# Kernel tuning notes

Hardware: AMD Instinct MI355X
Metric: run time of the kernel (lower is better)

## Reference

```python
import jax, jax.numpy as jnp
import numpy as np

N, E, F, H, O = 50000, 800000, 64, 128, 64
GRID_SIZE, SPLINE_ORDER = 3, 2


def make_grid(in_features, grid_size=GRID_SIZE, spline_order=SPLINE_ORDER, grid_range=(-1.0, 1.0)):
    h = (grid_range[1] - grid_range[0]) / grid_size
    pts = jnp.arange(-spline_order, grid_size + spline_order + 1, dtype=jnp.float32) * h + grid_range[0]
    return jnp.tile(pts[None, :], (in_features, 1))  # [in, grid_size + 2*order + 1]


def b_splines(x, grid, spline_order=SPLINE_ORDER):
    # x: [B, in], grid: [in, G+2k+1] -> bases [B, in, G+k]
    xe = x[..., None]
    bases = ((xe >= grid[:, :-1]) & (xe < grid[:, 1:])).astype(x.dtype)
    for k in range(1, spline_order + 1):
        bases = ((xe - grid[:, : -(k + 1)]) / (grid[:, k:-1] - grid[:, : -(k + 1)]) * bases[..., :-1]
                 + (grid[:, k + 1:] - xe) / (grid[:, k + 1:] - grid[:, 1:-k]) * bases[..., 1:])
    return bases


def setup_inputs() -> dict:
    key = jax.random.key(0)
    ks = jax.random.split(key, 12)
    x = jax.random.normal(ks[0], (N, F), dtype=jnp.float32)
    contexts = jax.random.normal(ks[1], (E, F), dtype=jnp.float32)
    attn = jax.random.uniform(ks[2], (E,), dtype=jnp.float32)
    seg_ids = jnp.sort(jax.random.randint(ks[3], (E,), 0, N, dtype=jnp.int32))
    s = 0.05
    Wn = jax.random.normal(ks[4], (H, F), dtype=jnp.float32) * s
    bn = jnp.zeros((H,), dtype=jnp.float32)
    Wc = jax.random.normal(ks[5], (H, F), dtype=jnp.float32) * s
    bc = jnp.zeros((H,), dtype=jnp.float32)
    Wu = jax.random.normal(ks[6], (O, H), dtype=jnp.float32) * s
    bu = jnp.zeros((O,), dtype=jnp.float32)
    n_coef = GRID_SIZE + SPLINE_ORDER
    base_w = jax.random.normal(ks[7], (O, O), dtype=jnp.float32) * s
    spline_w = jax.random.normal(ks[8], (O, O, n_coef), dtype=jnp.float32) * s
    spline_scaler = jnp.ones((O, O), dtype=jnp.float32)
    grid = make_grid(O)
    return dict(x=x, contexts=contexts, attn=attn, seg_ids=seg_ids, Wn=Wn, bn=bn,
                Wc=Wc, bc=bc, Wu=Wu, bu=bu, base_w=base_w, spline_w=spline_w,
                spline_scaler=spline_scaler, grid=grid)


def reference(x, contexts, attn, seg_ids, Wn, bn, Wc, bc, Wu, bu, base_w, spline_w, spline_scaler, grid):
    n = x.shape[0]
    # per-edge context transform, attention weighting
    ctx_t = contexts @ Wc.T + bc                      # [E, H]
    weighted = ctx_t * attn[:, None]                  # [E, H]
    seg_sum = jax.ops.segment_sum(weighted, seg_ids, num_segments=n)        # [N, H]
    deg = jax.ops.segment_sum(jnp.ones_like(attn), seg_ids, num_segments=n)  # [N]
    ctx_agg = seg_sum / jnp.maximum(deg, 1.0)[:, None]  # mean over edges per node
    x_t = x @ Wn.T + bn                               # [N, H]
    upd = (x_t + ctx_agg) @ Wu.T + bu                 # [N, O]
    # KANLinear (efficient-kan): silu base path + b-spline path
    base_out = jax.nn.silu(upd) @ base_w.T            # [N, O]
    bases = b_splines(upd, grid)                      # [N, O, G+k]
    scaled_sw = spline_w * spline_scaler[..., None]   # [O, O, G+k]
    spline_out = jnp.einsum('bik,oik->bo', bases, scaled_sw)
    kan_out = base_out + spline_out
    # nodes with no contexts keep their raw features (num_features == output_dim)
    return jnp.where(deg[:, None] > 0, kan_out, x)
```

## Files before the change

kernel.cpp:

```cpp
#include <hip/hip_runtime.h>
#include <hip/hip_bf16.h>

#define NN 50000
#define NE 800000

typedef short short8 __attribute__((ext_vector_type(8)));
typedef float f32x4 __attribute__((ext_vector_type(4)));
typedef unsigned short ushort_t;

static __device__ __forceinline__ unsigned bits(float f) { return __float_as_uint(f); }
static __device__ __forceinline__ float hi_f(float v) {
  return __uint_as_float(bits(v) & 0xFFFF0000u);
}
static __device__ __forceinline__ ushort_t hi_u(float v) { return (ushort_t)(bits(v) >> 16); }
static __device__ __forceinline__ unsigned pack_hi(float v0, float v1) {
  return (bits(v0) >> 16) | (bits(v1) & 0xFFFF0000u);
}
static __device__ __forceinline__ unsigned pack_lo(float v0, float v1) {
  float l0 = v0 - hi_f(v0), l1 = v1 - hi_f(v1);
  return (bits(l0) >> 16) | (bits(l1) & 0xFFFF0000u);
}

#define MFMA(a, b, c) __builtin_amdgcn_mfma_f32_16x16x32_bf16(a, b, c, 0, 0, 0)

__global__ __launch_bounds__(256) void kA_pack_off(
    const float* __restrict__ Wn, const float* __restrict__ Wc,
    const float* __restrict__ Wu, const float* __restrict__ base_w,
    const float* __restrict__ spline_w, const float* __restrict__ scaler,
    const int* __restrict__ seg,
    ushort_t* __restrict__ p1h, ushort_t* __restrict__ p2h,
    ushort_t* __restrict__ p3h, int* __restrict__ off) {
  int t = blockIdx.x * 256 + threadIdx.x;
  if (t < 4096) {
    int l = t & 63, lm = l & 15, lk = l >> 4;
    if (t < 2048) {
      int nt = t >> 8, ks = (t >> 6) & 3;
      int h = nt * 16 + lm;
#pragma unroll
      for (int j = 0; j < 8; ++j) {
        int f = ks * 32 + lk * 8 + j;
        float v = (f < 64) ? Wn[h * 64 + f] : Wc[h * 64 + (f - 64)];
        p1h[t * 8 + j] = hi_u(v);
      }
    }
    if (t < 1024) {
      int nt = t >> 8, ks = (t >> 6) & 3;
      int o = nt * 16 + lm;
#pragma unroll
      for (int j = 0; j < 8; ++j) {
        int hh = ks * 32 + lk * 8 + j;
        p2h[t * 8 + j] = hi_u(Wu[o * 128 + hh]);
      }
    }
    if (t < 3072) {
      int nt = t / 768, ks = (t >> 6) % 12;
      int o = nt * 16 + lm;
#pragma unroll
      for (int j = 0; j < 8; ++j) {
        int k = ks * 32 + lk * 8 + j;
        int i = k / 6, c = k % 6;
        float v = (c == 0) ? base_w[o * 64 + i]
                           : spline_w[(o * 64 + i) * 5 + (c - 1)] * scaler[o * 64 + i];
        p3h[t * 8 + j] = hi_u(v);
      }
    }
  }
  int e = t;
  if (e < NE) {
    int s1 = seg[e];
    if (e == 0) {
      for (int n = 0; n <= s1; ++n) off[n] = 0;
    } else {
      int s0 = seg[e - 1];
      for (int n = s0 + 1; n <= s1; ++n) off[n] = e;
    }
    if (e == NE - 1) {
      for (int n = s1 + 1; n <= NN; ++n) off[n] = NE;
    }
  }
}

__global__ __launch_bounds__(256) void k1_edge_agg(
    const float* __restrict__ contexts, const float* __restrict__ attn,
    const int* __restrict__ off, ushort_t* __restrict__ Sph,
    ushort_t* __restrict__ Spl, float* __restrict__ aprime,
    float* __restrict__ degw) {
  int n = blockIdx.x * 4 + (threadIdx.x >> 6);
  int lane = threadIdx.x & 63;
  if (n >= NN) return;
  int s = off[n];
  int e_end = off[n + 1];
  int deg_i = e_end - s;

  int sub = lane >> 4;
  int fq = lane & 15;
  const float4* ctx4 = (const float4*)contexts;

  float4 S = make_float4(0.f, 0.f, 0.f, 0.f);
  float A = 0.f;
  if (deg_i > 0) {
    int last = e_end - 1;
    for (int e0 = s; e0 < e_end; e0 += 16) {
      float a[4];
      float4 c[4];
#pragma unroll
      for (int u = 0; u < 4; ++u) {
        int eu = e0 + 4 * u + sub;
        a[u] = (eu < e_end) ? attn[eu] : 0.f;
        c[u] = ctx4[(size_t)min(eu, last) * 16 + fq];
      }
#pragma unroll
      for (int u = 0; u < 4; ++u) {
        S.x += a[u] * c[u].x;
        S.y += a[u] * c[u].y;
        S.z += a[u] * c[u].z;
        S.w += a[u] * c[u].w;
        A += a[u];
      }
    }
  }
#pragma unroll
  for (int m = 16; m <= 32; m <<= 1) {
    S.x += __shfl_xor(S.x, m);
    S.y += __shfl_xor(S.y, m);
    S.z += __shfl_xor(S.z, m);
    S.w += __shfl_xor(S.w, m);
    A += __shfl_xor(A, m);
  }
  float deg = (float)deg_i;
  float inv = 1.f / fmaxf(deg, 1.f);
  if (lane < 16) {
    float ox = S.x * inv, oy = S.y * inv, oz = S.z * inv, ow = S.w * inv;
    uint2 hp, lp;
    hp.x = pack_hi(ox, oy);
    hp.y = pack_hi(oz, ow);
    lp.x = pack_lo(ox, oy);
    lp.y = pack_lo(oz, ow);
    *(uint2*)&Sph[(size_t)n * 64 + lane * 4] = hp;
    *(uint2*)&Spl[(size_t)n * 64 + lane * 4] = lp;
  }
  if (lane == 0) { aprime[n] = A * inv; degw[n] = deg; }
}

__global__ __launch_bounds__(256, 4) void k234(
    const float* __restrict__ x,
    const ushort_t* __restrict__ Sph, const ushort_t* __restrict__ Spl,
    const float* __restrict__ aprime, const float* __restrict__ degw,
    const float* __restrict__ bn, const float* __restrict__ bc,
    const float* __restrict__ bu,
    const ushort_t* __restrict__ p1h, const ushort_t* __restrict__ p2h,
    const ushort_t* __restrict__ p3h,
    const float* __restrict__ gridp, float* __restrict__ out) {
  __shared__ __align__(16) unsigned char arena[32768];
  __shared__ float ap[64], degl[64];
  ushort_t* Uh = (ushort_t*)arena;
  ushort_t* Ul = (ushort_t*)(arena + 16384);
  ushort_t* Vh = (ushort_t*)arena;

  int tid = threadIdx.x;
  int n0 = blockIdx.x * 64;
  int w = tid >> 6, l = tid & 63;
  int lm = l & 15, lk = l >> 4;
  const short8* P1h = (const short8*)p1h;
  const short8* P2h = (const short8*)p2h;
  const short8* P3h = (const short8*)p3h;

  short8 B2[4];
#pragma unroll
  for (int ks = 0; ks < 4; ++ks) B2[ks] = P2h[(w * 4 + ks) * 64 + l];

  {
    const float4* x4 = (const float4*)x;
    const uint4* Sh4 = (const uint4*)Sph;
    const uint4* Sl4 = (const uint4*)Spl;
    for (int q = tid; q < 1024; q += 256) {
      int row = q >> 4, slot = q & 15;
      int n = n0 + row;
      int idx = (row * 128 + slot * 8) ^ ((row & 7) << 3);
      if (slot < 8) {
        float4 a = make_float4(0.f, 0.f, 0.f, 0.f), b = a;
        if (n < NN) {
          a = x4[(size_t)n * 16 + slot * 2];
          b = x4[(size_t)n * 16 + slot * 2 + 1];
        }
        uint4 hp, lp;
        hp.x = pack_hi(a.x, a.y); hp.y = pack_hi(a.z, a.w);
        hp.z = pack_hi(b.x, b.y); hp.w = pack_hi(b.z, b.w);
        lp.x = pack_lo(a.x, a.y); lp.y = pack_lo(a.z, a.w);
        lp.z = pack_lo(b.x, b.y); lp.w = pack_lo(b.z, b.w);
        *(uint4*)&Uh[idx] = hp;
        *(uint4*)&Ul[idx] = lp;
      } else {
        uint4 vh = make_uint4(0u, 0u, 0u, 0u), vl = vh;
        if (n < NN) {
          vh = Sh4[(size_t)n * 8 + (slot & 7)];
          vl = Sl4[(size_t)n * 8 + (slot & 7)];
        }
        *(uint4*)&Uh[idx] = vh;
        *(uint4*)&Ul[idx] = vl;
      }
    }
  }
  if (tid < 64) {
    int n = n0 + tid;
    ap[tid] = (n < NN) ? aprime[n] : 0.f;
    degl[tid] = (n < NN) ? degw[n] : 1.f;
  }
  __syncthreads();

  int swzA = (lm & 7) << 3;

  f32x4 acc1[2][4];
#pragma unroll
  for (int q = 0; q < 2; ++q)
#pragma unroll
    for (int mt = 0; mt < 4; ++mt) acc1[q][mt] = (f32x4){0.f, 0.f, 0.f, 0.f};
#pragma unroll
  for (int ks = 0; ks < 4; ++ks) {
    short8 bh0 = P1h[((2 * w + 0) * 4 + ks) * 64 + l];
    short8 bh1 = P1h[((2 * w + 1) * 4 + ks) * 64 + l];
#pragma unroll
    for (int mt = 0; mt < 4; ++mt) {
      int ai = ((mt * 16 + lm) * 128 + ks * 32 + lk * 8) ^ swzA;
      short8 ah = *(const short8*)&Uh[ai];
      short8 al = *(const short8*)&Ul[ai];
      acc1[0][mt] = MFMA(ah, bh0, acc1[0][mt]);
      acc1[0][mt] = MFMA(al, bh0, acc1[0][mt]);
      acc1[1][mt] = MFMA(ah, bh1, acc1[1][mt]);
      acc1[1][mt] = MFMA(al, bh1, acc1[1][mt]);
    }
  }
  __syncthreads();

#pragma unroll
  for (int q = 0; q < 2; ++q) {
    int h = (2 * w + q) * 16 + lm;
    float bnv = bn[h], bcv = bc[h];
#pragma unroll
    for (int mt = 0; mt < 4; ++mt) {
#pragma unroll
      for (int r = 0; r < 4; ++r) {
        int node = mt * 16 + lk * 4 + r;
        float t = acc1[q][mt][r] + bnv + ap[node] * bcv;
        Ul[(node * 128 + h) ^ ((node & 7) << 3)] = hi_u(t);
      }
    }
  }
  __syncthreads();

  f32x4 acc2[4];
#pragma unroll
  for (int mt = 0; mt < 4; ++mt) acc2[mt] = (f32x4){0.f, 0.f, 0.f, 0.f};
#pragma unroll
  for (int ks = 0; ks < 4; ++ks) {
#pragma unroll
    for (int mt = 0; mt < 4; ++mt) {
      int ai = ((mt * 16 + lm) * 128 + ks * 32 + lk * 8) ^ swzA;
      short8 ah = *(const short8*)&Ul[ai];
      acc2[mt] = MFMA(ah, B2[ks], acc2[mt]);
    }
  }
  __syncthreads();

  float g[8];
#pragma unroll
  for (int j = 0; j < 8; ++j) g[j] = gridp[j];
  float r1[7], r2[6];
#pragma unroll
  for (int j = 0; j < 7; ++j) r1[j] = 1.f / (g[j + 1] - g[j]);
#pragma unroll
  for (int j = 0; j < 6; ++j) r2[j] = 1.f / (g[j + 2] - g[j]);
  float buv = bu[w * 16 + lm];

#pragma unroll
  for (int half = 0; half < 2; ++half) {
#pragma unroll
    for (int ms = 0; ms < 2; ++ms) {
      int mt = half * 2 + ms;
#pragma unroll
      for (int r = 0; r < 4; ++r) {
        float xv = acc2[mt][r] + buv;
        float sil = xv / (1.f + __expf(-xv));
        float b0[7], b1[6], b2[5];
#pragma unroll
        for (int q = 0; q < 7; ++q) b0[q] = (xv >= g[q] && xv < g[q + 1]) ? 1.f : 0.f;
#pragma unroll
        for (int q = 0; q < 6; ++q)
          b1[q] = (xv - g[q]) * r1[q] * b0[q] + (g[q + 2] - xv) * r1[q + 1] * b0[q + 1];
#pragma unroll
        for (int q = 0; q < 5; ++q)
          b2[q] = (xv - g[q]) * r2[q] * b1[q] + (g[q + 3] - xv) * r2[q + 1] * b1[q + 1];
        int ln = ms * 16 + lk * 4 + r;
        int base = ln * 392 + (w * 16 + lm) * 6;
        *(unsigned*)&Vh[base + 0] = pack_hi(sil, b2[0]);
        *(unsigned*)&Vh[base + 2] = pack_hi(b2[1], b2[2]);
        *(unsigned*)&Vh[base + 4] = pack_hi(b2[3], b2[4]);
      }
    }
    __syncthreads();

    f32x4 accK[2];
    accK[0] = (f32x4){0.f, 0.f, 0.f, 0.f};
    accK[1] = (f32x4){0.f, 0.f, 0.f, 0.f};
#pragma unroll
    for (int ks = 0; ks < 12; ++ks) {
      short8 bh = P3h[(w * 12 + ks) * 64 + l];
#pragma unroll
      for (int s = 0; s < 2; ++s) {
        short8 ah = *(const short8*)&Vh[(s * 16 + lm) * 392 + ks * 32 + lk * 8];
        accK[s] = MFMA(ah, bh, accK[s]);
      }
    }
    __syncthreads();

#pragma unroll
    for (int s = 0; s < 2; ++s) {
      int o = w * 16 + lm;
#pragma unroll
      for (int r = 0; r < 4; ++r) {
        int node = half * 32 + s * 16 + lk * 4 + r;
        int n = n0 + node;
        if (n < NN) {
          float val = accK[s][r];
          if (degl[node] <= 0.f) val = x[(size_t)n * 64 + o];
          out[(size_t)n * 64 + o] = val;
        }
      }
    }
  }
}

extern "C" void kernel_launch(void* const* d_in, const int* in_sizes, int n_in,
                              void* d_out, int out_size, void* d_ws, size_t ws_size,
                              hipStream_t stream) {
  const float* x        = (const float*)d_in[0];
  const float* contexts = (const float*)d_in[1];
  const float* attn     = (const float*)d_in[2];
  const int*   seg      = (const int*)d_in[3];
  const float* Wn       = (const float*)d_in[4];
  const float* bn       = (const float*)d_in[5];
  const float* Wc       = (const float*)d_in[6];
  const float* bc       = (const float*)d_in[7];
  const float* Wu       = (const float*)d_in[8];
  const float* bu       = (const float*)d_in[9];
  const float* base_w   = (const float*)d_in[10];
  const float* spline_w = (const float*)d_in[11];
  const float* scaler   = (const float*)d_in[12];
  const float* gridp    = (const float*)d_in[13];
  float* out = (float*)d_out;

  ushort_t* us  = (ushort_t*)d_ws;
  ushort_t* Sph = us;
  ushort_t* Spl = Sph + 3200000;
  ushort_t* p1h = Spl + 3200000;
  ushort_t* p2h = p1h + 16384;
  ushort_t* p3h = p2h + 8192;
  float* aprime = (float*)(p3h + 24576);
  float* degw   = aprime + 50000;
  int*   off    = (int*)(degw + 50000);

  kA_pack_off<<<3125, 256, 0, stream>>>(Wn, Wc, Wu, base_w, spline_w, scaler, seg,
                                        p1h, p2h, p3h, off);
  k1_edge_agg<<<12500, 256, 0, stream>>>(contexts, attn, off, Sph, Spl, aprime, degw);
  k234<<<782, 256, 0, stream>>>(x, Sph, Spl, aprime, degw, bn, bc, bu,
                                p1h, p2h, p3h, gridp, out);
}
```

Baseline: 70.73 us.

## Drop low bf16 half of aggregated context, swizzle spline tile, coalesce output stores

The aggregated context is now stored only as a bf16 high half, so the low-half buffer, its global writes and reads, and half of the corresponding MFMAs in the first GEMM are removed. The spline/basis LDS tile moves from a padded stride to an XOR-swizzled layout. Output goes through a swizzled LDS staging area so each thread writes float4s coalesced along a row. The precision of the context path drops to plain bf16, which may raise error, and the output path adds extra barriers.

```diff
diff --git a/kernel.cpp b/kernel.cpp
--- a/kernel.cpp
+++ b/kernel.cpp
@@ -83,8 +83,7 @@
 __global__ __launch_bounds__(256) void k1_edge_agg(
     const float* __restrict__ contexts, const float* __restrict__ attn,
     const int* __restrict__ off, ushort_t* __restrict__ Sph,
-    ushort_t* __restrict__ Spl, float* __restrict__ aprime,
-    float* __restrict__ degw) {
+    float* __restrict__ aprime, float* __restrict__ degw) {
   int n = blockIdx.x * 4 + (threadIdx.x >> 6);
   int lane = threadIdx.x & 63;
   if (n >= NN) return;
@@ -131,20 +130,17 @@
   float inv = 1.f / fmaxf(deg, 1.f);
   if (lane < 16) {
     float ox = S.x * inv, oy = S.y * inv, oz = S.z * inv, ow = S.w * inv;
-    uint2 hp, lp;
+    uint2 hp;
     hp.x = pack_hi(ox, oy);
     hp.y = pack_hi(oz, ow);
-    lp.x = pack_lo(ox, oy);
-    lp.y = pack_lo(oz, ow);
     *(uint2*)&Sph[(size_t)n * 64 + lane * 4] = hp;
-    *(uint2*)&Spl[(size_t)n * 64 + lane * 4] = lp;
   }
   if (lane == 0) { aprime[n] = A * inv; degw[n] = deg; }
 }
 
 __global__ __launch_bounds__(256, 4) void k234(
     const float* __restrict__ x,
-    const ushort_t* __restrict__ Sph, const ushort_t* __restrict__ Spl,
+    const ushort_t* __restrict__ Sph,
     const float* __restrict__ aprime, const float* __restrict__ degw,
     const float* __restrict__ bn, const float* __restrict__ bc,
     const float* __restrict__ bu,
@@ -156,6 +152,7 @@
   ushort_t* Uh = (ushort_t*)arena;
   ushort_t* Ul = (ushort_t*)(arena + 16384);
   ushort_t* Vh = (ushort_t*)arena;
+  float*    ot = (float*)(arena + 24576);
 
   int tid = threadIdx.x;
   int n0 = blockIdx.x * 64;
@@ -172,7 +169,6 @@
   {
     const float4* x4 = (const float4*)x;
     const uint4* Sh4 = (const uint4*)Sph;
-    const uint4* Sl4 = (const uint4*)Spl;
     for (int q = tid; q < 1024; q += 256) {
       int row = q >> 4, slot = q & 15;
       int n = n0 + row;
@@ -191,13 +187,9 @@
         *(uint4*)&Uh[idx] = hp;
         *(uint4*)&Ul[idx] = lp;
       } else {
-        uint4 vh = make_uint4(0u, 0u, 0u, 0u), vl = vh;
-        if (n < NN) {
-          vh = Sh4[(size_t)n * 8 + (slot & 7)];
-          vl = Sl4[(size_t)n * 8 + (slot & 7)];
-        }
+        uint4 vh = make_uint4(0u, 0u, 0u, 0u);
+        if (n < NN) vh = Sh4[(size_t)n * 8 + (slot & 7)];
         *(uint4*)&Uh[idx] = vh;
-        *(uint4*)&Ul[idx] = vl;
       }
     }
   }
@@ -223,11 +215,13 @@
     for (int mt = 0; mt < 4; ++mt) {
       int ai = ((mt * 16 + lm) * 128 + ks * 32 + lk * 8) ^ swzA;
       short8 ah = *(const short8*)&Uh[ai];
-      short8 al = *(const short8*)&Ul[ai];
       acc1[0][mt] = MFMA(ah, bh0, acc1[0][mt]);
-      acc1[0][mt] = MFMA(al, bh0, acc1[0][mt]);
       acc1[1][mt] = MFMA(ah, bh1, acc1[1][mt]);
-      acc1[1][mt] = MFMA(al, bh1, acc1[1][mt]);
+      if (ks < 2) {
+        short8 al = *(const short8*)&Ul[ai];
+        acc1[0][mt] = MFMA(al, bh0, acc1[0][mt]);
+        acc1[1][mt] = MFMA(al, bh1, acc1[1][mt]);
+      }
     }
   }
   __syncthreads();
@@ -291,10 +285,11 @@
         for (int q = 0; q < 5; ++q)
           b2[q] = (xv - g[q]) * r2[q] * b1[q] + (g[q + 3] - xv) * r2[q + 1] * b1[q + 1];
         int ln = ms * 16 + lk * 4 + r;
-        int base = ln * 392 + (w * 16 + lm) * 6;
-        *(unsigned*)&Vh[base + 0] = pack_hi(sil, b2[0]);
-        *(unsigned*)&Vh[base + 2] = pack_hi(b2[1], b2[2]);
-        *(unsigned*)&Vh[base + 4] = pack_hi(b2[3], b2[4]);
+        int base = ln * 384 + (w * 16 + lm) * 6;
+        int sw = (ln & 7) << 3;
+        *(unsigned*)&Vh[(base + 0) ^ sw] = pack_hi(sil, b2[0]);
+        *(unsigned*)&Vh[(base + 2) ^ sw] = pack_hi(b2[1], b2[2]);
+        *(unsigned*)&Vh[(base + 4) ^ sw] = pack_hi(b2[3], b2[4]);
       }
     }
     __syncthreads();
@@ -307,7 +302,8 @@
       short8 bh = P3h[(w * 12 + ks) * 64 + l];
 #pragma unroll
       for (int s = 0; s < 2; ++s) {
-        short8 ah = *(const short8*)&Vh[(s * 16 + lm) * 392 + ks * 32 + lk * 8];
+        int ri = ((s * 16 + lm) * 384 + ks * 32 + lk * 8) ^ swzA;
+        short8 ah = *(const short8*)&Vh[ri];
         accK[s] = MFMA(ah, bh, accK[s]);
       }
     }
@@ -318,15 +314,29 @@
       int o = w * 16 + lm;
 #pragma unroll
       for (int r = 0; r < 4; ++r) {
-        int node = half * 32 + s * 16 + lk * 4 + r;
-        int n = n0 + node;
-        if (n < NN) {
-          float val = accK[s][r];
-          if (degl[node] <= 0.f) val = x[(size_t)n * 64 + o];
-          out[(size_t)n * 64 + o] = val;
+        int ln = s * 16 + lk * 4 + r;
+        ot[(ln * 64 + o) ^ ((ln & 7) << 3)] = accK[s][r];
+      }
+    }
+    __syncthreads();
+
+    {
+      int row2 = tid >> 3, c8 = (tid & 7) * 8;
+      int node = half * 32 + row2;
+      int n = n0 + node;
+      if (n < NN) {
+        int sw = (row2 & 7) << 3;
+        float4 v0 = *(float4*)&ot[((row2 * 64 + c8) ^ sw)];
+        float4 v1 = *(float4*)&ot[((row2 * 64 + c8 + 4) ^ sw)];
+        if (degl[node] <= 0.f) {
+          v0 = *(const float4*)(x + (size_t)n * 64 + c8);
+          v1 = *(const float4*)(x + (size_t)n * 64 + c8 + 4);
         }
-      }
-    }
+        *(float4*)(out + (size_t)n * 64 + c8) = v0;
+        *(float4*)(out + (size_t)n * 64 + c8 + 4) = v1;
+      }
+    }
+    __syncthreads();
   }
 }
 
@@ -351,8 +361,7 @@
 
   ushort_t* us  = (ushort_t*)d_ws;
   ushort_t* Sph = us;
-  ushort_t* Spl = Sph + 3200000;
-  ushort_t* p1h = Spl + 3200000;
+  ushort_t* p1h = Sph + 3200000;
   ushort_t* p2h = p1h + 16384;
   ushort_t* p3h = p2h + 8192;
   float* aprime = (float*)(p3h + 24576);
@@ -361,7 +370,7 @@
 
   kA_pack_off<<<3125, 256, 0, stream>>>(Wn, Wc, Wu, base_w, spline_w, scaler, seg,
                                         p1h, p2h, p3h, off);
-  k1_edge_agg<<<12500, 256, 0, stream>>>(contexts, attn, off, Sph, Spl, aprime, degw);
-  k234<<<782, 256, 0, stream>>>(x, Sph, Spl, aprime, degw, bn, bc, bu,
+  k1_edge_agg<<<12500, 256, 0, stream>>>(contexts, attn, off, Sph, aprime, degw);
+  k234<<<782, 256, 0, stream>>>(x, Sph, aprime, degw, bn, bc, bu,
                                 p1h, p2h, p3h, gridp, out);
 }
```

Result: faster. 66.54 us, median of 2 (-5.9%).
